# Kernel tuning notes

Hardware: AMD Instinct MI355X
Metric: run time of the kernel (lower is better)

## Reference

```python
import jax, jax.numpy as jnp
import numpy as np

B, N, M = 64, 1024, 4096
HID, OUT = 2048, 512

def setup_inputs() -> dict:
    key = jax.random.key(0)
    ks = jax.random.split(key, 10)
    s = 0.02  # weight init scale
    return {
        "pos": jax.random.normal(ks[0], (B, N, 3), dtype=jnp.float32),
        "basis": jax.random.normal(ks[1], (M, 3), dtype=jnp.float32),
        "W0": jax.random.normal(ks[2], (N, HID), dtype=jnp.float32) * s,
        "b0": jnp.zeros((HID,), dtype=jnp.float32),
        "W1": jax.random.normal(ks[3], (HID, HID), dtype=jnp.float32) * s,
        "b1": jnp.zeros((HID,), dtype=jnp.float32),
        "W2": jax.random.normal(ks[4], (HID, HID), dtype=jnp.float32) * s,
        "b2": jnp.zeros((HID,), dtype=jnp.float32),
        "W3": jax.random.normal(ks[5], (HID, OUT), dtype=jnp.float32) * s,
        "b3": jnp.zeros((OUT,), dtype=jnp.float32),
    }

def reference(pos, basis, W0, b0, W1, b1, W2, b2, W3, b3):
    # pairwise Euclidean distances: [B, N, M] via ||p||^2 + ||q||^2 - 2 p.q
    p2 = jnp.sum(pos * pos, axis=-1, keepdims=True)            # [B, N, 1]
    q2 = jnp.sum(basis * basis, axis=-1)                       # [M]
    pq = jnp.einsum('bnc,mc->bnm', pos, basis)                 # [B, N, M]
    d2 = p2 + q2[None, None, :] - 2.0 * pq
    dists = jnp.sqrt(jnp.maximum(d2, 1e-12))                   # [B, N, M]
    x = jnp.min(dists, axis=2)                                 # [B, N] -> MLP in_dim = N
    # MLP (eval mode: dropout identity, norm=None, plain last layer)
    x = jax.nn.relu(x @ W0 + b0)
    x = jax.nn.relu(x @ W1 + b1)
    x = jax.nn.relu(x @ W2 + b2)
    return x @ W3 + b3                                         # [B, OUT]
```

## Files before the change

kernel.cpp:

```cpp
#include <hip/hip_runtime.h>
#include <hip/hip_bf16.h>
#include <math.h>

#define B_SZ   64
#define N_SZ   1024
#define M_SZ   4096
#define HID_SZ 2048
#define OUT_SZ 512

#define AS1 __attribute__((address_space(1)))
#define AS3 __attribute__((address_space(3)))

__global__ __launch_bounds__(256, 2) void dist_min_kernel(
    const float* __restrict__ pos,
    const float* __restrict__ basis,
    float* __restrict__ xT)
{
  const int tid  = threadIdx.x;
  const int lane = tid & 63;
  const int wave = tid >> 6;

  float nqx[16], nqy[16], nqz[16], qc[16];
#pragma unroll
  for (int i = 0; i < 16; ++i) {
    int j = wave * 1024 + i * 64 + lane;
    float qx = basis[3*j+0], qy = basis[3*j+1], qz = basis[3*j+2];
    nqx[i] = -qx; nqy[i] = -qy; nqz[i] = -qz;
    qc[i]  = 0.5f * (qx*qx + qy*qy + qz*qz);
  }

  __shared__ float red[16][256];

  const int pbase = blockIdx.x * 128;

  for (int c = 0; c < 8; ++c) {
    const int cbase = pbase + c * 16;
    const float* pp = pos + (size_t)3 * cbase;
    float pc[48];
#pragma unroll
    for (int e = 0; e < 48; ++e) pc[e] = pp[e];

#pragma unroll
    for (int p = 0; p < 16; ++p) {
      const float px = pc[3*p+0], py = pc[3*p+1], pz = pc[3*p+2];
      float t[16];
#pragma unroll
      for (int i = 0; i < 16; ++i) t[i] = fmaf(nqx[i], px, qc[i]);
#pragma unroll
      for (int i = 0; i < 16; ++i) t[i] = fmaf(nqy[i], py, t[i]);
#pragma unroll
      for (int i = 0; i < 16; ++i) t[i] = fmaf(nqz[i], pz, t[i]);
      float m0 = fminf(fminf(t[0],  t[1]),  t[2]);
      float m1 = fminf(fminf(t[3],  t[4]),  t[5]);
      float m2 = fminf(fminf(t[6],  t[7]),  t[8]);
      float m3 = fminf(fminf(t[9],  t[10]), t[11]);
      float m4 = fminf(fminf(t[12], t[13]), t[14]);
      float r0 = fminf(fminf(m0, m1), m2);
      float r1 = fminf(fminf(m3, m4), t[15]);
      red[p][tid] = fminf(r0, r1);
    }
    __syncthreads();

    {
      const int p   = tid >> 4;
      const int sub = tid & 15;
      const float4* r4 = (const float4*)&red[p][sub * 16];
      float4 v0 = r4[0], v1 = r4[1], v2 = r4[2], v3 = r4[3];
      float w0 = fminf(fminf(v0.x, v0.y), fminf(v0.z, v0.w));
      float w1 = fminf(fminf(v1.x, v1.y), fminf(v1.z, v1.w));
      float w2 = fminf(fminf(v2.x, v2.y), fminf(v2.z, v2.w));
      float w3 = fminf(fminf(v3.x, v3.y), fminf(v3.z, v3.w));
      float v  = fminf(fminf(w0, w1), fminf(w2, w3));
#pragma unroll
      for (int o = 1; o < 16; o <<= 1) v = fminf(v, __shfl_xor(v, o));
      if (sub == 0) {
        int i = cbase + p;
        float px = pos[3*i+0], py = pos[3*i+1], pz = pos[3*i+2];
        float p2 = px*px + py*py + pz*pz;
        float d2 = fmaf(2.f, v, p2);
        d2 = fmaxf(d2, 1e-12f);
        int n = i & (N_SZ - 1);
        int b = i >> 10;
        xT[n * 64 + b] = sqrtf(d2);
      }
    }
    __syncthreads();
  }
}

template <int J, int KSPAN>
__global__ __launch_bounds__(256, 2) void gemm3_kernel(
    const float* __restrict__ xT,
    const float* __restrict__ W,
    float* __restrict__ P)
{
  constexpr int NS = KSPAN / 16;
  const int jt   = blockIdx.x;
  const int s    = blockIdx.y;
  const int tid  = threadIdx.x;
  const int lane = tid & 63;
  const int wave = tid >> 6;
  const int jl = lane & 15;
  const int bq = lane >> 4;
  const int j0 = jt * 64 + jl * 4;
  const int b0 = wave * 16 + bq * 4;

  __shared__ __align__(16) float xs[KSPAN][64];
  __shared__ __align__(16) float wring[2][16][64];

  const float* wsrc = W + ((size_t)s * KSPAN + wave * 4 + (lane >> 4)) * J
                        + jt * 64 + (lane & 15) * 4;

  {
    const float4* src4 = (const float4*)(xT + (size_t)s * KSPAN * 64);
    float4* dst4 = (float4*)&xs[0][0];
    constexpr int NITER = KSPAN / 16;
#pragma unroll
    for (int i = 0; i < NITER; ++i)
      dst4[i * 256 + tid] = src4[i * 256 + tid];
  }
  __builtin_amdgcn_global_load_lds(
      (const AS1 void*)wsrc,
      (AS3 void*)&wring[0][wave * 4][0], 16, 0, 0);
  asm volatile("s_waitcnt vmcnt(0)" ::: "memory");
  __syncthreads();

  float acc[4][4];
#pragma unroll
  for (int a = 0; a < 4; ++a)
#pragma unroll
    for (int c = 0; c < 4; ++c) acc[a][c] = 0.f;

#pragma unroll 1
  for (int t = 0; t < NS; ++t) {
    const int buf = t & 1;
    if (t + 1 < NS) {
      __builtin_amdgcn_global_load_lds(
          (const AS1 void*)(wsrc + (size_t)(t + 1) * 16 * J),
          (AS3 void*)&wring[buf ^ 1][wave * 4][0], 16, 0, 0);
    }
#pragma unroll
    for (int r = 0; r < 16; ++r) {
      float4 w4 = *(const float4*)&wring[buf][r][jl * 4];
      float4 x4 = *(const float4*)&xs[t * 16 + r][b0];
      const float wv[4] = {w4.x, w4.y, w4.z, w4.w};
      const float xv[4] = {x4.x, x4.y, x4.z, x4.w};
#pragma unroll
      for (int a = 0; a < 4; ++a)
#pragma unroll
        for (int c = 0; c < 4; ++c)
          acc[a][c] = fmaf(xv[a], wv[c], acc[a][c]);
    }
    asm volatile("s_waitcnt vmcnt(0)" ::: "memory");
    __syncthreads();
  }

#pragma unroll
  for (int c = 0; c < 4; ++c) {
    float4 o = make_float4(acc[0][c], acc[1][c], acc[2][c], acc[3][c]);
    *(float4*)(P + ((size_t)s * J + (j0 + c)) * 64 + b0) = o;
  }
}

template <int J, int KS, bool RELU, bool TRANS>
__global__ __launch_bounds__(256) void reduce_bias_kernel(
    const float* __restrict__ P,
    const float* __restrict__ bias,
    float* __restrict__ out)
{
  const int t = blockIdx.x * 256 + threadIdx.x;
  const int b = t & 63;
  const int j = t >> 6;
  float v = 0.f;
#pragma unroll
  for (int s = 0; s < KS; ++s) v += P[((size_t)s * J + j) * 64 + b];
  v += bias[j];
  if (RELU) v = fmaxf(v, 0.f);
  if (TRANS) out[j * 64 + b] = v;
  else       out[(size_t)b * J + j] = v;
}

extern "C" void kernel_launch(void* const* d_in, const int* in_sizes, int n_in,
                              void* d_out, int out_size, void* d_ws, size_t ws_size,
                              hipStream_t stream) {
  const float* pos   = (const float*)d_in[0];
  const float* basis = (const float*)d_in[1];
  const float* W0    = (const float*)d_in[2];
  const float* b0    = (const float*)d_in[3];
  const float* W1    = (const float*)d_in[4];
  const float* b1    = (const float*)d_in[5];
  const float* W2    = (const float*)d_in[6];
  const float* b2    = (const float*)d_in[7];
  const float* W3    = (const float*)d_in[8];
  const float* b3    = (const float*)d_in[9];
  float* out = (float*)d_out;

  char* ws = (char*)d_ws;
  float* P  = (float*)ws;
  float* xA = (float*)(ws + (8u << 20));
  float* xB = (float*)(ws + (8u << 20) + (512u << 10));

  dist_min_kernel<<<512, 256, 0, stream>>>(pos, basis, xA);

  gemm3_kernel<HID_SZ, 64>
      <<<dim3(HID_SZ / 64, 1024 / 64), 256, 0, stream>>>(xA, W0, P);
  reduce_bias_kernel<HID_SZ, 16, true, true>
      <<<HID_SZ * 64 / 256, 256, 0, stream>>>(P, b0, xB);

  gemm3_kernel<HID_SZ, 128>
      <<<dim3(HID_SZ / 64, 2048 / 128), 256, 0, stream>>>(xB, W1, P);
  reduce_bias_kernel<HID_SZ, 16, true, true>
      <<<HID_SZ * 64 / 256, 256, 0, stream>>>(P, b1, xA);

  gemm3_kernel<HID_SZ, 128>
      <<<dim3(HID_SZ / 64, 2048 / 128), 256, 0, stream>>>(xA, W2, P);
  reduce_bias_kernel<HID_SZ, 16, true, true>
      <<<HID_SZ * 64 / 256, 256, 0, stream>>>(P, b2, xB);

  gemm3_kernel<OUT_SZ, 32>
      <<<dim3(OUT_SZ / 64, 2048 / 32), 256, 0, stream>>>(xB, W3, P);
  reduce_bias_kernel<OUT_SZ, 64, false, false>
      <<<OUT_SZ * 64 / 256, 256, 0, stream>>>(P, b3, out);
}
```

Measured before the change: 199.3 us.

## Fuse MLP layers into one persistent kernel with software grid barriers

Replaces the eight separate GEMM and reduce launches with a single persistent 256-block kernel that runs every layer's split-K GEMM and bias/ReLU reduction, separated by atomic-counter grid barriers. Split-K drops from 16 slices to 8 (32 for the last layer), so each block covers a larger K range in 128-row chunks, and the grid matches the CU count. The aim is to remove launch gaps and tail effects between small kernels. In exchange it adds barrier spin overhead, relies on all 256 blocks being co-resident, and gives each layer less parallelism per block.

```diff
diff --git a/kernel.cpp b/kernel.cpp
--- a/kernel.cpp
+++ b/kernel.cpp
@@ -11,6 +11,12 @@
 #define AS1 __attribute__((address_space(1)))
 #define AS3 __attribute__((address_space(3)))
 
+#define NBLK 256
+
+__global__ void init_kernel(unsigned* bar) {
+  if (threadIdx.x < 2) bar[threadIdx.x] = 0u;
+}
+
 __global__ __launch_bounds__(256, 2) void dist_min_kernel(
     const float* __restrict__ pos,
     const float* __restrict__ basis,
@@ -30,7 +36,6 @@
   }
 
   __shared__ float red[16][256];
-
   const int pbase = blockIdx.x * 128;
 
   for (int c = 0; c < 8; ++c) {
@@ -88,43 +93,45 @@
   }
 }
 
-template <int J, int KSPAN>
-__global__ __launch_bounds__(256, 2) void gemm3_kernel(
-    const float* __restrict__ xT,
+__device__ __forceinline__ void grid_barrier(unsigned* cnt, unsigned* gen) {
+  __syncthreads();
+  if (threadIdx.x == 0) {
+    __threadfence();
+    unsigned g = atomicAdd(gen, 0u);
+    unsigned a = atomicAdd(cnt, 1u);
+    if (a == NBLK - 1u) {
+      atomicExch(cnt, 0u);
+      __threadfence();
+      atomicAdd(gen, 1u);
+    } else {
+      while (atomicAdd(gen, 0u) == g) __builtin_amdgcn_s_sleep(2);
+    }
+    __threadfence();
+  }
+  __syncthreads();
+}
+
+template <int K, int J, int JT, int SLICES>
+__device__ __forceinline__ void gemm_phase(
+    const float* __restrict__ xin,
     const float* __restrict__ W,
-    float* __restrict__ P)
-{
-  constexpr int NS = KSPAN / 16;
-  const int jt   = blockIdx.x;
-  const int s    = blockIdx.y;
+    float* __restrict__ P,
+    float* xs, float* wring)
+{
+  constexpr int KSPAN = K / SLICES;
+  constexpr int HALF  = (KSPAN > 128) ? 128 : KSPAN;
+  constexpr int NH    = KSPAN / HALF;
+  constexpr int NS    = HALF / 16;
   const int tid  = threadIdx.x;
   const int lane = tid & 63;
   const int wave = tid >> 6;
   const int jl = lane & 15;
   const int bq = lane >> 4;
+  const int jt = blockIdx.x % JT;
+  const int s  = blockIdx.x / JT;
   const int j0 = jt * 64 + jl * 4;
   const int b0 = wave * 16 + bq * 4;
 
-  __shared__ __align__(16) float xs[KSPAN][64];
-  __shared__ __align__(16) float wring[2][16][64];
-
-  const float* wsrc = W + ((size_t)s * KSPAN + wave * 4 + (lane >> 4)) * J
-                        + jt * 64 + (lane & 15) * 4;
-
-  {
-    const float4* src4 = (const float4*)(xT + (size_t)s * KSPAN * 64);
-    float4* dst4 = (float4*)&xs[0][0];
-    constexpr int NITER = KSPAN / 16;
-#pragma unroll
-    for (int i = 0; i < NITER; ++i)
-      dst4[i * 256 + tid] = src4[i * 256 + tid];
-  }
-  __builtin_amdgcn_global_load_lds(
-      (const AS1 void*)wsrc,
-      (AS3 void*)&wring[0][wave * 4][0], 16, 0, 0);
-  asm volatile("s_waitcnt vmcnt(0)" ::: "memory");
-  __syncthreads();
-
   float acc[4][4];
 #pragma unroll
   for (int a = 0; a < 4; ++a)
@@ -132,27 +139,44 @@
     for (int c = 0; c < 4; ++c) acc[a][c] = 0.f;
 
 #pragma unroll 1
-  for (int t = 0; t < NS; ++t) {
-    const int buf = t & 1;
-    if (t + 1 < NS) {
-      __builtin_amdgcn_global_load_lds(
-          (const AS1 void*)(wsrc + (size_t)(t + 1) * 16 * J),
-          (AS3 void*)&wring[buf ^ 1][wave * 4][0], 16, 0, 0);
-    }
-#pragma unroll
-    for (int r = 0; r < 16; ++r) {
-      float4 w4 = *(const float4*)&wring[buf][r][jl * 4];
-      float4 x4 = *(const float4*)&xs[t * 16 + r][b0];
-      const float wv[4] = {w4.x, w4.y, w4.z, w4.w};
-      const float xv[4] = {x4.x, x4.y, x4.z, x4.w};
-#pragma unroll
-      for (int a = 0; a < 4; ++a)
-#pragma unroll
-        for (int c = 0; c < 4; ++c)
-          acc[a][c] = fmaf(xv[a], wv[c], acc[a][c]);
-    }
+  for (int h = 0; h < NH; ++h) {
+    const int kbase = s * KSPAN + h * HALF;
+    {
+      const float4* sx = (const float4*)(xin + (size_t)kbase * 64);
+      float4* dx = (float4*)xs;
+#pragma unroll
+      for (int i = 0; i < HALF / 16; ++i)
+        dx[i * 256 + tid] = sx[i * 256 + tid];
+    }
+    const float* wsrc = W + ((size_t)(kbase + wave * 4 + (lane >> 4))) * J
+                          + jt * 64 + (lane & 15) * 4;
+    __builtin_amdgcn_global_load_lds((const AS1 void*)wsrc,
+                                     (AS3 void*)(wring + wave * 256), 16, 0, 0);
     asm volatile("s_waitcnt vmcnt(0)" ::: "memory");
     __syncthreads();
+
+#pragma unroll 1
+    for (int t = 0; t < NS; ++t) {
+      const int buf = t & 1;
+      if (t + 1 < NS)
+        __builtin_amdgcn_global_load_lds(
+            (const AS1 void*)(wsrc + (size_t)(t + 1) * 16 * J),
+            (AS3 void*)(wring + (buf ^ 1) * 1024 + wave * 256), 16, 0, 0);
+#pragma unroll
+      for (int r = 0; r < 16; ++r) {
+        float4 w4 = *(const float4*)(wring + buf * 1024 + r * 64 + jl * 4);
+        float4 x4 = *(const float4*)(xs + (t * 16 + r) * 64 + b0);
+        const float wv[4] = {w4.x, w4.y, w4.z, w4.w};
+        const float xv[4] = {x4.x, x4.y, x4.z, x4.w};
+#pragma unroll
+        for (int a = 0; a < 4; ++a)
+#pragma unroll
+          for (int c = 0; c < 4; ++c)
+            acc[a][c] = fmaf(xv[a], wv[c], acc[a][c]);
+      }
+      asm volatile("s_waitcnt vmcnt(0)" ::: "memory");
+      __syncthreads();
+    }
   }
 
 #pragma unroll
@@ -162,22 +186,53 @@
   }
 }
 
-template <int J, int KS, bool RELU, bool TRANS>
-__global__ __launch_bounds__(256) void reduce_bias_kernel(
-    const float* __restrict__ P,
-    const float* __restrict__ bias,
+template <int J, int SLICES, bool RELU, bool FINAL>
+__device__ __forceinline__ void reduce_phase(
+    const float* __restrict__ P, const float* __restrict__ bias,
     float* __restrict__ out)
 {
-  const int t = blockIdx.x * 256 + threadIdx.x;
-  const int b = t & 63;
-  const int j = t >> 6;
-  float v = 0.f;
-#pragma unroll
-  for (int s = 0; s < KS; ++s) v += P[((size_t)s * J + j) * 64 + b];
-  v += bias[j];
-  if (RELU) v = fmaxf(v, 0.f);
-  if (TRANS) out[j * 64 + b] = v;
-  else       out[(size_t)b * J + j] = v;
+  constexpr int TOT = J * 64;
+#pragma unroll 1
+  for (int idx = blockIdx.x * 256 + threadIdx.x; idx < TOT; idx += NBLK * 256) {
+    const int b = idx & 63;
+    const int j = idx >> 6;
+    float v = 0.f;
+#pragma unroll
+    for (int s = 0; s < SLICES; ++s) v += P[((size_t)s * J + j) * 64 + b];
+    v += bias[j];
+    if (RELU) v = fmaxf(v, 0.f);
+    if (FINAL) out[(size_t)b * J + j] = v;
+    else       out[idx] = v;
+  }
+}
+
+__global__ __launch_bounds__(256, 1) void mlp_fused_kernel(
+    const float* __restrict__ x0,
+    const float* __restrict__ W0, const float* __restrict__ bb0,
+    const float* __restrict__ W1, const float* __restrict__ bb1,
+    const float* __restrict__ W2, const float* __restrict__ bb2,
+    const float* __restrict__ W3, const float* __restrict__ bb3,
+    float* __restrict__ P, float* __restrict__ xh0, float* __restrict__ xh1,
+    unsigned* bar, float* __restrict__ out)
+{
+  __shared__ __align__(16) float xs[128 * 64];
+  __shared__ __align__(16) float wring[2 * 16 * 64];
+
+  gemm_phase<1024, 2048, 32, 8>(x0, W0, P, xs, wring);
+  grid_barrier(bar, bar + 1);
+  reduce_phase<2048, 8, true, false>(P, bb0, xh0);
+  grid_barrier(bar, bar + 1);
+  gemm_phase<2048, 2048, 32, 8>(xh0, W1, P, xs, wring);
+  grid_barrier(bar, bar + 1);
+  reduce_phase<2048, 8, true, false>(P, bb1, xh1);
+  grid_barrier(bar, bar + 1);
+  gemm_phase<2048, 2048, 32, 8>(xh1, W2, P, xs, wring);
+  grid_barrier(bar, bar + 1);
+  reduce_phase<2048, 8, true, false>(P, bb2, xh0);
+  grid_barrier(bar, bar + 1);
+  gemm_phase<2048, 512, 8, 32>(xh0, W3, P, xs, wring);
+  grid_barrier(bar, bar + 1);
+  reduce_phase<512, 32, false, true>(P, bb3, out);
 }
 
 extern "C" void kernel_launch(void* const* d_in, const int* in_sizes, int n_in,
@@ -196,29 +251,14 @@
   float* out = (float*)d_out;
 
   char* ws = (char*)d_ws;
-  float* P  = (float*)ws;
-  float* xA = (float*)(ws + (8u << 20));
-  float* xB = (float*)(ws + (8u << 20) + (512u << 10));
-
-  dist_min_kernel<<<512, 256, 0, stream>>>(pos, basis, xA);
-
-  gemm3_kernel<HID_SZ, 64>
-      <<<dim3(HID_SZ / 64, 1024 / 64), 256, 0, stream>>>(xA, W0, P);
-  reduce_bias_kernel<HID_SZ, 16, true, true>
-      <<<HID_SZ * 64 / 256, 256, 0, stream>>>(P, b0, xB);
-
-  gemm3_kernel<HID_SZ, 128>
-      <<<dim3(HID_SZ / 64, 2048 / 128), 256, 0, stream>>>(xB, W1, P);
-  reduce_bias_kernel<HID_SZ, 16, true, true>
-      <<<HID_SZ * 64 / 256, 256, 0, stream>>>(P, b1, xA);
-
-  gemm3_kernel<HID_SZ, 128>
-      <<<dim3(HID_SZ / 64, 2048 / 128), 256, 0, stream>>>(xA, W2, P);
-  reduce_bias_kernel<HID_SZ, 16, true, true>
-      <<<HID_SZ * 64 / 256, 256, 0, stream>>>(P, b2, xB);
-
-  gemm3_kernel<OUT_SZ, 32>
-      <<<dim3(OUT_SZ / 64, 2048 / 32), 256, 0, stream>>>(xB, W3, P);
-  reduce_bias_kernel<OUT_SZ, 64, false, false>
-      <<<OUT_SZ * 64 / 256, 256, 0, stream>>>(P, b3, out);
-}
+  float*    P   = (float*)ws;
+  float*    xh0 = (float*)(ws + (4u << 20));
+  float*    xh1 = (float*)(ws + (4u << 20) + (512u << 10));
+  float*    x0  = (float*)(ws + (5u << 20));
+  unsigned* bar = (unsigned*)(ws + (6u << 20));
+
+  init_kernel<<<1, 64, 0, stream>>>(bar);
+  dist_min_kernel<<<512, 256, 0, stream>>>(pos, basis, x0);
+  mlp_fused_kernel<<<NBLK, 256, 0, stream>>>(
+      x0, W0, b0, W1, b1, W2, b2, W3, b3, P, xh0, xh1, bar, out);
+}
```

New measurement: 375.9 us. 88.6% more time.
